# Kernel optimization log

Hardware: AMD Instinct MI355X
Metric: run time of the kernel (lower is better)

The kernel has to match this reference:

```python
import jax, jax.numpy as jnp
import numpy as np
import math
from jax import lax

B, HS, WS, C, T, TD, HH, TOPM = 8, 64, 64, 512, 77, 512, 8, 3
DH = C // HH
CONF_TH = 0.35


def _layernorm(x, w, b, eps=1e-5):
    mu = x.mean(-1, keepdims=True)
    var = ((x - mu) ** 2).mean(-1, keepdims=True)
    return (x - mu) * lax.rsqrt(var + eps) * w + b


def _l2norm(x, eps=1e-6):
    n = jnp.sqrt((x * x).sum(-1, keepdims=True))
    return x / jnp.maximum(n, eps)


def _forward(visual_features, text_features, geo_mask,
             ln1_w, ln1_b, wq, bq, wk, bk, wv, bv, wo, bo,
             gate_w, gate_b, logit_scale, alpha,
             ln2_w, ln2_b, ffn_w1, ffn_b1, ffn_w2, ffn_b2):
    Bb, Hs, Ws, Cv = visual_features.shape
    N = Hs * Ws
    # Pre-LN + flatten spatial
    x = _layernorm(visual_features, ln1_w, ln1_b).reshape(Bb, N, Cv)
    q_full = x @ wq + bq                                  # [B,N,C]
    pad_mask = jnp.abs(text_features).sum(-1) <= 1e-6     # [B,T]
    k_full = text_features @ wk + bk                      # [B,T,C]
    v_full = text_features @ wv + bv
    # per-token L2 normalize over full channel dim, then split heads
    q = _l2norm(q_full).reshape(Bb, N, HH, DH)
    k = _l2norm(k_full).reshape(Bb, T, HH, DH)
    v = v_full.reshape(Bb, T, HH, DH)
    scale = jnp.exp(jnp.clip(logit_scale, -2.0, 2.0)) / jnp.sqrt(jnp.float32(DH))
    sim = jnp.einsum('bnhd,bthd->bnht', q, k) * scale     # [B,N,H,T]
    # geo gate (4D tensor branch): log-bias on logits + multiplicative channel gate later
    gate_map = jnp.clip(geo_mask, 0.3, 1.0)               # [B,1,Hs,Ws]
    geo_gate_flat = gate_map.reshape(Bb, N, 1)            # [B,N,1]
    sim = sim + jnp.log(jnp.maximum(gate_map.reshape(Bb, N), 1e-6))[:, :, None, None]
    sim = jnp.where(pad_mask[:, None, None, :], -jnp.inf, sim)
    # Top-K sparsification before softmax (threshold at the K-th value)
    topv = lax.top_k(sim, TOPM)[0]                        # [B,N,H,K]
    sim = jnp.where(sim >= topv[..., -1:], sim, -jnp.inf)
    attn = jax.nn.softmax(sim, axis=-1)
    attn = attn / jnp.maximum(attn.sum(-1, keepdims=True), 1e-6)
    # fully-padded rows -> zero
    all_pad = pad_mask.all(axis=1)
    attn = jnp.where(all_pad[:, None, None, None], 0.0, attn)
    # confidence bypass: conf = max_prob * (1 - normalized entropy), mean over heads
    a_hn = attn.transpose(0, 2, 1, 3)                     # [B,H,N,T]
    maxp = a_hn.max(-1, keepdims=True)
    t_eff = jnp.maximum((a_hn > 0).astype(a_hn.dtype).sum(-1, keepdims=True), 2.0)
    p = jnp.maximum(a_hn, 1e-8)
    ent = jnp.maximum(-(p * jnp.log(p)).sum(-1, keepdims=True) / jnp.log(t_eff), 0.0)
    conf = jnp.clip(maxp * (1.0 - ent), 0.0, 1.0).mean(axis=1)   # [B,N,1]
    conf_scale = CONF_TH + (1.0 - CONF_TH) * jnp.clip(conf, 0.0, 1.0)
    aligned = jnp.einsum('bnht,bthd->bnhd', attn, v).reshape(Bb, N, HH * DH)
    aligned = (aligned @ wo + bo) * conf_scale
    gate = jax.nn.sigmoid(x @ gate_w + gate_b) * geo_gate_flat
    y = x + alpha * gate * aligned
    h = _layernorm(y, ln2_w, ln2_b)
    y = y + (jax.nn.gelu(h @ ffn_w1 + ffn_b1, approximate=False) @ ffn_w2 + ffn_b2)
    return y.reshape(Bb, Hs, Ws, Cv)


def setup_inputs() -> dict:
    key = jax.random.key(0)
    ks = jax.random.split(key, 16)
    def w(k, shp, fan_in):
        return (jax.random.normal(k, shp, jnp.float32) * (1.0 / math.sqrt(fan_in))).astype(jnp.float32)
    return {
        'visual_features': jax.random.normal(ks[0], (B, HS, WS, C), jnp.float32),
        'text_features':   jax.random.normal(ks[1], (B, T, TD), jnp.float32),
        'geo_mask':        jax.random.uniform(ks[2], (B, 1, HS, WS), jnp.float32),
        'ln1_w': jnp.ones((C,), jnp.float32), 'ln1_b': jnp.zeros((C,), jnp.float32),
        'wq': w(ks[3], (C, C), C),   'bq': jnp.zeros((C,), jnp.float32),
        'wk': w(ks[4], (TD, C), TD), 'bk': jnp.zeros((C,), jnp.float32),
        'wv': w(ks[5], (TD, C), TD), 'bv': jnp.zeros((C,), jnp.float32),
        'wo': w(ks[6], (C, C), C),   'bo': jnp.zeros((C,), jnp.float32),
        'gate_w': w(ks[7], (C, C), C), 'gate_b': jnp.zeros((C,), jnp.float32),
        'logit_scale': jnp.float32(math.log(1.0 / 0.07)),
        'alpha': jnp.float32(0.1),
        'ln2_w': jnp.ones((C,), jnp.float32), 'ln2_b': jnp.zeros((C,), jnp.float32),
        'ffn_w1': w(ks[8], (C, 4 * C), C),    'ffn_b1': jnp.zeros((4 * C,), jnp.float32),
        'ffn_w2': w(ks[9], (4 * C, C), 4 * C), 'ffn_b2': jnp.zeros((C,), jnp.float32),
    }


def reference(visual_features, text_features, geo_mask,
              ln1_w, ln1_b, wq, bq, wk, bk, wv, bv, wo, bo,
              gate_w, gate_b, logit_scale, alpha,
              ln2_w, ln2_b, ffn_w1, ffn_b1, ffn_w2, ffn_b2):
    return _forward(visual_features, text_features, geo_mask,
                    ln1_w, ln1_b, wq, bq, wk, bk, wv, bv, wo, bo,
                    gate_w, gate_b, logit_scale, alpha,
                    ln2_w, ln2_b, ffn_w1, ffn_b1, ffn_w2, ffn_b2)
```

## Files before the change

kernel.cpp:

```cpp
#include <hip/hip_runtime.h>
#include <hip/hip_bf16.h>
#include <math.h>

#define TT 77
#define MTOT 32768

typedef __attribute__((ext_vector_type(8))) short bf16x8;
typedef __attribute__((ext_vector_type(4))) float floatx4;

#define GPTR(p) ((const __attribute__((address_space(1))) void*)(p))
#define LPTR(p) ((__attribute__((address_space(3))) void*)(p))

__device__ __forceinline__ float wred_sum(float v) {
#pragma unroll
  for (int o = 32; o >= 1; o >>= 1) v += __shfl_xor(v, o, 64);
  return v;
}

__device__ __forceinline__ unsigned short f2bf(float f) {
  unsigned int u = __float_as_uint(f);
  unsigned int r = (u + 0x7fffu + ((u >> 16) & 1u)) >> 16;
  return (unsigned short)r;
}
__device__ __forceinline__ float bf2f(unsigned short h) {
  return __uint_as_float(((unsigned int)h) << 16);
}

__device__ __forceinline__ float fast_gelu(float o) {
  const float z = fabsf(o) * 0.70710678118654752f;
  const float t = __builtin_amdgcn_rcpf(fmaf(0.3275911f, z, 1.0f));
  float p = fmaf(1.061405429f, t, -1.453152027f);
  p = fmaf(p, t, 1.421413741f);
  p = fmaf(p, t, -0.284496736f);
  p = fmaf(p, t, 0.254829592f);
  p = p * t;
  const float erfz = fmaf(-p, __expf(-z * z), 1.0f);
  const float s = __builtin_copysignf(erfz, o);
  return 0.5f * o * (1.0f + s);
}

__device__ __forceinline__ float fast_sigmoid(float o) {
  return __builtin_amdgcn_rcpf(1.0f + __expf(-o));
}

__global__ __launch_bounds__(256)
void ln_bf16_kernel(const float* __restrict__ in, const float* __restrict__ gw,
                    const float* __restrict__ gb, unsigned short* __restrict__ out) {
  const int wv = threadIdx.x >> 6, lane = threadIdx.x & 63;
  const size_t row = (size_t)blockIdx.x * 4 + wv;
  const float* p = in + row * 512 + lane * 8;
  float4 a = *(const float4*)p;
  float4 b = *(const float4*)(p + 4);
  float s = a.x + a.y + a.z + a.w + b.x + b.y + b.z + b.w;
  float mu = wred_sum(s) * (1.0f / 512.0f);
  float d[8] = {a.x - mu, a.y - mu, a.z - mu, a.w - mu,
                b.x - mu, b.y - mu, b.z - mu, b.w - mu};
  float ss = 0.f;
#pragma unroll
  for (int i = 0; i < 8; ++i) ss = fmaf(d[i], d[i], ss);
  float var = wred_sum(ss) * (1.0f / 512.0f);
  float rstd = rsqrtf(var + 1e-5f);
  float4 w0 = *(const float4*)(gw + lane * 8);
  float4 w1 = *(const float4*)(gw + lane * 8 + 4);
  float4 c0 = *(const float4*)(gb + lane * 8);
  float4 c1 = *(const float4*)(gb + lane * 8 + 4);
  float o[8];
  o[0] = d[0] * rstd * w0.x + c0.x;  o[1] = d[1] * rstd * w0.y + c0.y;
  o[2] = d[2] * rstd * w0.z + c0.z;  o[3] = d[3] * rstd * w0.w + c0.w;
  o[4] = d[4] * rstd * w1.x + c1.x;  o[5] = d[5] * rstd * w1.y + c1.y;
  o[6] = d[6] * rstd * w1.z + c1.z;  o[7] = d[7] * rstd * w1.w + c1.w;
  __align__(16) unsigned short ob[8];
#pragma unroll
  for (int i = 0; i < 8; ++i) ob[i] = f2bf(o[i]);
  *(uint4*)(out + row * 512 + lane * 8) = *(const uint4*)ob;
}

__global__ __launch_bounds__(256)
void qnorm_kernel(const float* __restrict__ q, const float* __restrict__ logit_scale,
                  unsigned short* __restrict__ qnb) {
  const int wv = threadIdx.x >> 6, lane = threadIdx.x & 63;
  const size_t row = (size_t)blockIdx.x * 4 + wv;
  const float ls = fminf(fmaxf(logit_scale[0], -2.0f), 2.0f);
  const float scale = expf(ls) * 0.125f;
  const float* p = q + row * 512 + lane * 8;
  float4 a = *(const float4*)p;
  float4 b = *(const float4*)(p + 4);
  float ss = a.x * a.x + a.y * a.y + a.z * a.z + a.w * a.w +
             b.x * b.x + b.y * b.y + b.z * b.z + b.w * b.w;
  ss = wred_sum(ss);
  const float nsc = scale / fmaxf(sqrtf(ss), 1e-6f);
  float o[8] = {a.x * nsc, a.y * nsc, a.z * nsc, a.w * nsc,
                b.x * nsc, b.y * nsc, b.z * nsc, b.w * nsc};
  __align__(16) unsigned short ob[8];
#pragma unroll
  for (int i = 0; i < 8; ++i) ob[i] = f2bf(o[i]);
  *(uint4*)(qnb + row * 512 + lane * 8) = *(const uint4*)ob;
}

__global__ __launch_bounds__(256)
void transpose_bf16_kernel(const float* __restrict__ W, unsigned short* __restrict__ WTb,
                           int K, int N) {
  __shared__ float s[32][33];
  const int tx = threadIdx.x & 31, ty = threadIdx.x >> 5;
  const int n0 = blockIdx.x * 32, k0 = blockIdx.y * 32;
#pragma unroll
  for (int j = 0; j < 4; ++j)
    s[ty + 8 * j][tx] = W[(size_t)(k0 + ty + 8 * j) * N + n0 + tx];
  __syncthreads();
#pragma unroll
  for (int j = 0; j < 4; ++j)
    WTb[(size_t)(n0 + ty + 8 * j) * K + k0 + tx] = f2bf(s[tx][ty + 8 * j]);
}

__global__ __launch_bounds__(256)
void transpose_pair_kernel(const float* __restrict__ W,
                           unsigned short* __restrict__ WTh,
                           unsigned short* __restrict__ WTl, int K, int N) {
  __shared__ float s[32][33];
  const int tx = threadIdx.x & 31, ty = threadIdx.x >> 5;
  const int n0 = blockIdx.x * 32, k0 = blockIdx.y * 32;
#pragma unroll
  for (int j = 0; j < 4; ++j)
    s[ty + 8 * j][tx] = W[(size_t)(k0 + ty + 8 * j) * N + n0 + tx];
  __syncthreads();
#pragma unroll
  for (int j = 0; j < 4; ++j) {
    const float a = s[tx][ty + 8 * j];
    const unsigned short hi = f2bf(a);
    WTh[(size_t)(n0 + ty + 8 * j) * K + k0 + tx] = hi;
    WTl[(size_t)(n0 + ty + 8 * j) * K + k0 + tx] = f2bf(a - bf2f(hi));
  }
}

__global__ __launch_bounds__(256)
void text_cvt_kernel(const float* __restrict__ text,
                     unsigned short* __restrict__ thi,
                     unsigned short* __restrict__ tlo,
                     float* __restrict__ negm) {
  const int wv = threadIdx.x >> 6, lane = threadIdx.x & 63;
  const int row = blockIdx.x * 4 + wv;
  if (row >= 616) {
    const uint4 z = {0u, 0u, 0u, 0u};
    *(uint4*)(thi + (size_t)row * 512 + lane * 8) = z;
    *(uint4*)(tlo + (size_t)row * 512 + lane * 8) = z;
    return;
  }
  const float* p = text + (size_t)row * 512 + lane * 8;
  float4 a = *(const float4*)p;
  float4 b = *(const float4*)(p + 4);
  float v[8] = {a.x, a.y, a.z, a.w, b.x, b.y, b.z, b.w};
  float ab = 0.f;
#pragma unroll
  for (int i = 0; i < 8; ++i) ab += fabsf(v[i]);
  ab = wred_sum(ab);
  __align__(16) unsigned short hb[8];
  __align__(16) unsigned short lb[8];
#pragma unroll
  for (int i = 0; i < 8; ++i) {
    hb[i] = f2bf(v[i]);
    lb[i] = f2bf(v[i] - bf2f(hb[i]));
  }
  *(uint4*)(thi + (size_t)row * 512 + lane * 8) = *(const uint4*)hb;
  *(uint4*)(tlo + (size_t)row * 512 + lane * 8) = *(const uint4*)lb;
  if (lane == 0) {
    const int bb = row / 77, t = row - bb * 77;
    negm[bb * 80 + t] = (ab <= 1e-6f) ? -INFINITY : 0.0f;
  }
}

__global__ __launch_bounds__(256)
void kv_gemm(const unsigned short* __restrict__ AH,
             const unsigned short* __restrict__ AL,
             const unsigned short* __restrict__ BH,
             const unsigned short* __restrict__ BL,
             const float* __restrict__ bk, const float* __restrict__ bv,
             float* __restrict__ outp) {
  const int K = 512;
  __shared__ __align__(16) unsigned short AsH[128 * 32];
  __shared__ __align__(16) unsigned short AsL[128 * 32];
  __shared__ __align__(16) unsigned short BsH[128 * 32];
  __shared__ __align__(16) unsigned short BsL[128 * 32];
  const int tid = threadIdx.x;
  const int wid = tid >> 6, lane = tid & 63;
  const int wr = wid >> 1, wc = wid & 1;
  const int m16 = lane & 15, quad = lane >> 4;
  const int row0 = blockIdx.y * 128, col0 = blockIdx.x * 128;

  const floatx4 zero4 = {0.f, 0.f, 0.f, 0.f};
  floatx4 acc[4][4];
#pragma unroll
  for (int i = 0; i < 4; ++i)
#pragma unroll
    for (int j = 0; j < 4; ++j) acc[i][j] = zero4;

  const int srow = tid >> 2;
  const int schunk = (tid & 3) ^ (srow & 3);
  const unsigned short* AgH = AH + (size_t)(row0 + srow) * K + schunk * 8;
  const unsigned short* AgL = AL + (size_t)(row0 + srow) * K + schunk * 8;
  const unsigned short* BgH = BH + (size_t)(col0 + srow) * K + schunk * 8;
  const unsigned short* BgL = BL + (size_t)(col0 + srow) * K + schunk * 8;
  char* AsHB = (char*)AsH + tid * 16;
  char* AsLB = (char*)AsL + tid * 16;
  char* BsHB = (char*)BsH + tid * 16;
  char* BsLB = (char*)BsL + tid * 16;
  const int rq = quad ^ (m16 & 3);
  const int aOfs = (wr * 64 + m16) * 32 + rq * 8;
  const int bOfs = (wc * 64 + m16) * 32 + rq * 8;

  for (int k0 = 0; k0 < K; k0 += 32) {
    __syncthreads();
    __builtin_amdgcn_global_load_lds(GPTR(AgH + k0), LPTR(AsHB), 16, 0, 0);
    __builtin_amdgcn_global_load_lds(GPTR(AgH + (size_t)64 * K + k0), LPTR(AsHB + 4096), 16, 0, 0);
    __builtin_amdgcn_global_load_lds(GPTR(AgL + k0), LPTR(AsLB), 16, 0, 0);
    __builtin_amdgcn_global_load_lds(GPTR(AgL + (size_t)64 * K + k0), LPTR(AsLB + 4096), 16, 0, 0);
    __builtin_amdgcn_global_load_lds(GPTR(BgH + k0), LPTR(BsHB), 16, 0, 0);
    __builtin_amdgcn_global_load_lds(GPTR(BgH + (size_t)64 * K + k0), LPTR(BsHB + 4096), 16, 0, 0);
    __builtin_amdgcn_global_load_lds(GPTR(BgL + k0), LPTR(BsLB), 16, 0, 0);
    __builtin_amdgcn_global_load_lds(GPTR(BgL + (size_t)64 * K + k0), LPTR(BsLB + 4096), 16, 0, 0);
    __syncthreads();
    bf16x8 afH[4], afL[4], bfH[4], bfL[4];
#pragma unroll
    for (int i = 0; i < 4; ++i) {
      afH[i] = *(const bf16x8*)(AsH + aOfs + i * 16 * 32);
      afL[i] = *(const bf16x8*)(AsL + aOfs + i * 16 * 32);
      bfH[i] = *(const bf16x8*)(BsH + bOfs + i * 16 * 32);
      bfL[i] = *(const bf16x8*)(BsL + bOfs + i * 16 * 32);
    }
#pragma unroll
    for (int mi = 0; mi < 4; ++mi)
#pragma unroll
      for (int ni = 0; ni < 4; ++ni) {
        acc[mi][ni] = __builtin_amdgcn_mfma_f32_16x16x32_bf16(afH[mi], bfH[ni], acc[mi][ni], 0, 0, 0);
        acc[mi][ni] = __builtin_amdgcn_mfma_f32_16x16x32_bf16(afH[mi], bfL[ni], acc[mi][ni], 0, 0, 0);
        acc[mi][ni] = __builtin_amdgcn_mfma_f32_16x16x32_bf16(afL[mi], bfH[ni], acc[mi][ni], 0, 0, 0);
      }
  }

  const float* bp = (col0 < 512) ? bk : bv;
  const int cbase = (col0 < 512) ? col0 : col0 - 512;
  float bb[4];
#pragma unroll
  for (int ni = 0; ni < 4; ++ni) bb[ni] = bp[cbase + wc * 64 + ni * 16 + m16];
#pragma unroll
  for (int mi = 0; mi < 4; ++mi)
#pragma unroll
    for (int r = 0; r < 4; ++r) {
      const int row = row0 + wr * 64 + mi * 16 + quad * 4 + r;
#pragma unroll
      for (int ni = 0; ni < 4; ++ni) {
        const int col = col0 + wc * 64 + ni * 16 + m16;
        outp[(size_t)row * 1024 + col] = acc[mi][ni][r] + bb[ni];
      }
    }
}

__global__ __launch_bounds__(256)
void knorm_kernel(const float* __restrict__ KV,
                  unsigned short* __restrict__ khb) {
  const int wv = threadIdx.x >> 6, lane = threadIdx.x & 63;
  const int row = blockIdx.x * 4 + wv;
  const float* p = KV + (size_t)row * 1024 + lane * 8;
  float4 a = *(const float4*)p;
  float4 b = *(const float4*)(p + 4);
  float v[8] = {a.x, a.y, a.z, a.w, b.x, b.y, b.z, b.w};
  float ss = 0.f;
#pragma unroll
  for (int i = 0; i < 8; ++i) ss = fmaf(v[i], v[i], ss);
  ss = wred_sum(ss);
  const float sc = 1.0f / fmaxf(sqrtf(ss), 1e-6f);
  const int bb = row / 77, t = row - bb * 77;
  const int c = lane * 8, h = c >> 6, d = c & 63;
  __align__(16) unsigned short ob[8];
#pragma unroll
  for (int i = 0; i < 8; ++i) ob[i] = f2bf(v[i] * sc);
  *(uint4*)(khb + (((size_t)bb * 8 + h) * 80 + t) * 64 + d) = *(const uint4*)ob;
}

__global__ __launch_bounds__(256)
void kpad_zero_kernel(unsigned short* __restrict__ khb, float* __restrict__ negm) {
  const int i = blockIdx.x * 256 + threadIdx.x;
  const int bh = i / 192, rem = i - bh * 192;
  const int t = 77 + rem / 64, d = rem & 63;
  khb[(((size_t)bh) * 80 + t) * 64 + d] = 0;
  if (i < 24) negm[(i / 3) * 80 + 77 + (i % 3)] = -INFINITY;
}

__global__ __launch_bounds__(256)
void sim_kernel(const unsigned short* __restrict__ qnb,
                const unsigned short* __restrict__ khb,
                const float* __restrict__ negm,
                float* __restrict__ SIM) {
  __shared__ __align__(16) unsigned short As[128 * 72];
  __shared__ __align__(16) unsigned short Bs[80 * 72];
  const int bh = blockIdx.y;
  const int b = bh >> 3, h = bh & 7;
  const int row0 = blockIdx.x * 128;
  const int tid = threadIdx.x;
  {
    const int r = tid >> 1, half = tid & 1;
    const unsigned short* src = qnb + ((size_t)b * 4096 + row0 + r) * 512 + h * 64 + half * 32;
    unsigned short* dst = As + r * 72 + half * 32;
    *(uint4*)dst = *(const uint4*)src;
    *(uint4*)(dst + 8) = *(const uint4*)(src + 8);
    *(uint4*)(dst + 16) = *(const uint4*)(src + 16);
    *(uint4*)(dst + 24) = *(const uint4*)(src + 24);
  }
  if (tid < 160) {
    const int r = tid >> 1, half = tid & 1;
    const unsigned short* src = khb + ((size_t)bh * 80 + r) * 64 + half * 32;
    unsigned short* dst = Bs + r * 72 + half * 32;
    *(uint4*)dst = *(const uint4*)src;
    *(uint4*)(dst + 8) = *(const uint4*)(src + 8);
    *(uint4*)(dst + 16) = *(const uint4*)(src + 16);
    *(uint4*)(dst + 24) = *(const uint4*)(src + 24);
  }
  __syncthreads();
  const int w = tid >> 6, lane = tid & 63;
  const int m16 = lane & 15, quad = lane >> 4;
  const unsigned short* aBase = As + (w * 32 + m16) * 72 + quad * 8;
  const unsigned short* bBase = Bs + m16 * 72 + quad * 8;
  bf16x8 af[2][2], bf[5][2];
#pragma unroll
  for (int mi = 0; mi < 2; ++mi)
#pragma unroll
    for (int kk = 0; kk < 2; ++kk)
      af[mi][kk] = *(const bf16x8*)(aBase + mi * 16 * 72 + kk * 32);
#pragma unroll
  for (int ni = 0; ni < 5; ++ni)
#pragma unroll
    for (int kk = 0; kk < 2; ++kk)
      bf[ni][kk] = *(const bf16x8*)(bBase + ni * 16 * 72 + kk * 32);
  const floatx4 zero4 = {0.f, 0.f, 0.f, 0.f};
  floatx4 acc[2][5];
#pragma unroll
  for (int mi = 0; mi < 2; ++mi)
#pragma unroll
    for (int ni = 0; ni < 5; ++ni) acc[mi][ni] = zero4;
#pragma unroll
  for (int kk = 0; kk < 2; ++kk)
#pragma unroll
    for (int mi = 0; mi < 2; ++mi)
#pragma unroll
      for (int ni = 0; ni < 5; ++ni)
        acc[mi][ni] = __builtin_amdgcn_mfma_f32_16x16x32_bf16(af[mi][kk], bf[ni][kk], acc[mi][ni], 0, 0, 0);
  float nm[5];
#pragma unroll
  for (int ni = 0; ni < 5; ++ni) nm[ni] = negm[b * 80 + ni * 16 + m16];
  float* obase = SIM + ((size_t)bh * 4096 + row0 + w * 32 + quad * 4) * 80 + m16;
#pragma unroll
  for (int mi = 0; mi < 2; ++mi)
#pragma unroll
    for (int ni = 0; ni < 5; ++ni)
#pragma unroll
      for (int r = 0; r < 4; ++r)
        obase[(size_t)(mi * 16 + r) * 80 + ni * 16] = acc[mi][ni][r] + nm[ni];
}

__global__ __launch_bounds__(256)
void attn_topk_pv_kernel(const float* __restrict__ SIM,
                         const float* __restrict__ vf,
                         unsigned short* __restrict__ alignedb,
                         float* __restrict__ conf_out) {
  const int g = blockIdx.x * 256 + threadIdx.x;
  const int b = g >> 15;
  const int local = g & 32767;
  const int n = local >> 3, h = local & 7;
  const float* sp = SIM + ((size_t)(b * 8 + h) * 4096 + n) * 80;

  float m1 = -INFINITY, m2 = -INFINITY, m3 = -INFINITY, m4 = -INFINITY;
  int a1 = 0, a2 = 0, a3 = 0;
#pragma unroll
  for (int i = 0; i < 20; ++i) {
    const float4 q = ((const float4*)sp)[i];
#pragma unroll
    for (int j = 0; j < 4; ++j) {
      const float v = (j == 0) ? q.x : (j == 1) ? q.y : (j == 2) ? q.z : q.w;
      const int t = i * 4 + j;
      const bool c1 = v > m1, c2 = v > m2, c3 = v > m3, c4 = v > m4;
      m4 = c4 ? (c3 ? m3 : v) : m4;
      m3 = c3 ? (c2 ? m2 : v) : m3;
      a3 = c3 ? (c2 ? a2 : t) : a3;
      m2 = c2 ? (c1 ? m1 : v) : m2;
      a2 = c2 ? (c1 ? a1 : t) : a2;
      m1 = c1 ? v : m1;
      a1 = c1 ? t : a1;
    }
  }

  const bool dead = (m1 == -INFINITY);
  if (dead) m1 = 0.0f;
  const bool tie = (!dead) && ((m1 == m2) || (m2 == m3) || (m3 == m4));

  const float d2 = m2 - m1, d3 = m3 - m1;
  const float e2 = __expf(d2), e3 = __expf(d3);
  float s0 = 1.0f + e2 + e3;
  float s1 = ((e2 > 0.f) ? e2 * d2 : 0.f) + ((e3 > 0.f) ? e3 * d3 : 0.f);
  float cntf = 1.0f + ((e2 > 0.f) ? 1.f : 0.f) + ((e3 > 0.f) ? 1.f : 0.f);

  const float w1 = dead ? 0.f : 1.f;
  const float* v1p = vf + (size_t)(b * 77 + a1) * 1024 + h * 64;
  const float* v2p = vf + (size_t)(b * 77 + a2) * 1024 + h * 64;
  const float* v3p = vf + (size_t)(b * 77 + a3) * 1024 + h * 64;
  float4 acc[16];
#pragma unroll
  for (int i = 0; i < 16; ++i) {
    const float4 x1 = ((const float4*)v1p)[i];
    const float4 x2 = ((const float4*)v2p)[i];
    const float4 x3 = ((const float4*)v3p)[i];
    float4 r;
    r.x = fmaf(e3, x3.x, fmaf(e2, x2.x, w1 * x1.x));
    r.y = fmaf(e3, x3.y, fmaf(e2, x2.y, w1 * x1.y));
    r.z = fmaf(e3, x3.z, fmaf(e2, x2.z, w1 * x1.z));
    r.w = fmaf(e3, x3.w, fmaf(e2, x2.w, w1 * x1.w));
    acc[i] = r;
  }

  if (__any(tie)) {
    if (tie) {
      s0 = 0.f; s1 = 0.f; cntf = 0.f;
#pragma unroll
      for (int i = 0; i < 16; ++i) acc[i] = (float4){0.f, 0.f, 0.f, 0.f};
      for (int t = 0; t < 80; ++t) {
        const float v = sp[t];
        if (v >= m3) {
          const float e = expf(v - m1);
          if (e > 0.f) {
            s0 += e; s1 = fmaf(e, v - m1, s1); cntf += 1.f;
            const float4* vp = (const float4*)(vf + (size_t)(b * 77 + t) * 1024 + h * 64);
#pragma unroll
            for (int i = 0; i < 16; ++i) {
              const float4 x = vp[i];
              acc[i].x = fmaf(e, x.x, acc[i].x);
              acc[i].y = fmaf(e, x.y, acc[i].y);
              acc[i].z = fmaf(e, x.z, acc[i].z);
              acc[i].w = fmaf(e, x.w, acc[i].w);
            }
          }
        }
      }
    }
  }

  const float inv = 1.0f / s0;
  const float entn = (__logf(s0) - s1 * inv) + (77.0f - cntf) * 1.8420681e-7f;
  const float ent = fmaxf(entn / __logf(fmaxf(cntf, 2.0f)), 0.0f);
  float conf_h = fminf(fmaxf(inv * (1.0f - ent), 0.0f), 1.0f);
  if (dead) conf_h = 0.f;
  float cs = conf_h;
  cs += __shfl_xor(cs, 1, 64);
  cs += __shfl_xor(cs, 2, 64);
  cs += __shfl_xor(cs, 4, 64);
  if (h == 0) {
    const float cm = fminf(fmaxf(cs * 0.125f, 0.0f), 1.0f);
    conf_out[(size_t)b * 4096 + n] = 0.35f + 0.65f * cm;
  }

  unsigned short* op = alignedb + ((size_t)b * 4096 + n) * 512 + h * 64;
#pragma unroll
  for (int i = 0; i < 8; ++i) {
    const float4 lo = acc[2 * i], hi = acc[2 * i + 1];
    uint4 pk;
    pk.x = (unsigned int)f2bf(lo.x * inv) | ((unsigned int)f2bf(lo.y * inv) << 16);
    pk.y = (unsigned int)f2bf(lo.z * inv) | ((unsigned int)f2bf(lo.w * inv) << 16);
    pk.z = (unsigned int)f2bf(hi.x * inv) | ((unsigned int)f2bf(hi.y * inv) << 16);
    pk.w = (unsigned int)f2bf(hi.z * inv) | ((unsigned int)f2bf(hi.w * inv) << 16);
    *(uint4*)(op + i * 8) = pk;
  }
}

template <int EPI>
__global__ __launch_bounds__(256)
void mfma_gemm(const unsigned short* __restrict__ A,
               const unsigned short* __restrict__ WT,
               const float* __restrict__ bias,
               void* __restrict__ outv, int M, int N, int K,
               const unsigned short* __restrict__ e0b,
               const float* __restrict__ e1f,
               const float* __restrict__ e2f,
               const float* __restrict__ scf) {
  __shared__ __align__(16) unsigned short As[128 * 32];
  __shared__ __align__(16) unsigned short Bs[128 * 32];
  const int tid = threadIdx.x;
  const int wid = tid >> 6, lane = tid & 63;
  const int wr = wid >> 1, wc = wid & 1;
  const int m16 = lane & 15, quad = lane >> 4;

  const int nwg = gridDim.x * gridDim.y;
  const int orig = blockIdx.y * gridDim.x + blockIdx.x;
  const int qq = nwg >> 3, rr = nwg & 7;
  const int xcd = orig & 7, base = orig >> 3;
  const int logical = (xcd < rr ? xcd * (qq + 1) : rr * (qq + 1) + (xcd - rr) * qq) + base;
  const int bx = logical % gridDim.x, by = logical / gridDim.x;
  const int row0 = by * 128, col0 = bx * 128;

  const floatx4 zero4 = {0.f, 0.f, 0.f, 0.f};
  floatx4 acc[4][4];
#pragma unroll
  for (int i = 0; i < 4; ++i)
#pragma unroll
    for (int j = 0; j < 4; ++j) acc[i][j] = zero4;

  const int srow = tid >> 2;
  const int schunk = (tid & 3) ^ (srow & 3);
  const unsigned short* Ag = A + (size_t)(row0 + srow) * K + schunk * 8;
  const unsigned short* Bg = WT + (size_t)(col0 + srow) * K + schunk * 8;
  char* AsB = (char*)As + tid * 16;
  char* BsB = (char*)Bs + tid * 16;
  const int rq = quad ^ (m16 & 3);
  const unsigned short* aP = As + (wr * 64 + m16) * 32 + rq * 8;
  const unsigned short* bP = Bs + (wc * 64 + m16) * 32 + rq * 8;

  for (int k0 = 0; k0 < K; k0 += 32) {
    __syncthreads();
    __builtin_amdgcn_global_load_lds(GPTR(Ag + k0), LPTR(AsB), 16, 0, 0);
    __builtin_amdgcn_global_load_lds(GPTR(Ag + (size_t)64 * K + k0), LPTR(AsB + 4096), 16, 0, 0);
    __builtin_amdgcn_global_load_lds(GPTR(Bg + k0), LPTR(BsB), 16, 0, 0);
    __builtin_amdgcn_global_load_lds(GPTR(Bg + (size_t)64 * K + k0), LPTR(BsB + 4096), 16, 0, 0);
    __syncthreads();
    bf16x8 af[4], bfr[4];
#pragma unroll
    for (int i = 0; i < 4; ++i) {
      af[i] = *(const bf16x8*)(aP + i * 16 * 32);
      bfr[i] = *(const bf16x8*)(bP + i * 16 * 32);
    }
#pragma unroll
    for (int mi = 0; mi < 4; ++mi)
#pragma unroll
      for (int ni = 0; ni < 4; ++ni)
        acc[mi][ni] = __builtin_amdgcn_mfma_f32_16x16x32_bf16(af[mi], bfr[ni], acc[mi][ni], 0, 0, 0);
  }

  float* outf = (float*)outv;
  unsigned short* outb = (unsigned short*)outv;
  const unsigned short* albf = (const unsigned short*)e1f;
  float bb[4];
#pragma unroll
  for (int ni = 0; ni < 4; ++ni) bb[ni] = bias[col0 + wc * 64 + ni * 16 + m16];
  const float alphav = (EPI == 2) ? scf[0] : 0.f;

#pragma unroll
  for (int mi = 0; mi < 4; ++mi) {
#pragma unroll
    for (int r = 0; r < 4; ++r) {
      const int row = row0 + wr * 64 + mi * 16 + quad * 4 + r;
      float rowscale = 1.f, geo = 0.f;
      if (EPI == 1) rowscale = e1f[row];
      if (EPI == 2) geo = fminf(fmaxf(e2f[row], 0.3f), 1.0f);
#pragma unroll
      for (int ni = 0; ni < 4; ++ni) {
        const int col = col0 + wc * 64 + ni * 16 + m16;
        const size_t idx = (size_t)row * N + col;
        float o = acc[mi][ni][r] + bb[ni];
        if (EPI == 0) {
          outf[idx] = o;
        } else if (EPI == 1) {
          outb[idx] = f2bf(o * rowscale);
        } else if (EPI == 2) {
          const float x = bf2f(e0b[idx]);
          const float al = bf2f(albf[idx]);
          const float sg = fast_sigmoid(o);
          outf[idx] = x + alphav * sg * geo * al;
        } else if (EPI == 3) {
          outb[idx] = f2bf(fast_gelu(o));
        } else {
          outf[idx] = o + e1f[idx];
        }
      }
    }
  }
}

extern "C" void kernel_launch(void* const* d_in, const int* in_sizes, int n_in,
                              void* d_out, int out_size, void* d_ws, size_t ws_size,
                              hipStream_t stream) {
  const float* visual = (const float*)d_in[0];
  const float* text   = (const float*)d_in[1];
  const float* geo    = (const float*)d_in[2];
  const float* ln1_w  = (const float*)d_in[3];
  const float* ln1_b  = (const float*)d_in[4];
  const float* wq     = (const float*)d_in[5];
  const float* bq     = (const float*)d_in[6];
  const float* wk     = (const float*)d_in[7];
  const float* bk     = (const float*)d_in[8];
  const float* wvw    = (const float*)d_in[9];
  const float* bv     = (const float*)d_in[10];
  const float* wo     = (const float*)d_in[11];
  const float* bo     = (const float*)d_in[12];
  const float* gate_w = (const float*)d_in[13];
  const float* gate_b = (const float*)d_in[14];
  const float* logit_scale = (const float*)d_in[15];
  const float* alpha  = (const float*)d_in[16];
  const float* ln2_w  = (const float*)d_in[17];
  const float* ln2_b  = (const float*)d_in[18];
  const float* ffn_w1 = (const float*)d_in[19];
  const float* ffn_b1 = (const float*)d_in[20];
  const float* ffn_w2 = (const float*)d_in[21];
  const float* ffn_b2 = (const float*)d_in[22];
  float* out = (float*)d_out;

  char* ws = (char*)d_ws;
  float* R0            = (float*)ws;
  float* BUF2          = (float*)(ws + 88080384);
  unsigned short* Xb   = (unsigned short*)(ws + 155189248);
  unsigned short* QNb  = (unsigned short*)(ws + 188743680);
  unsigned short* wqT  = (unsigned short*)(ws + 222298112);
  unsigned short* woT  = wqT + 262144;
  unsigned short* gateT = woT + 262144;
  unsigned short* w1T  = gateT + 262144;
  unsigned short* w2T  = w1T + 1048576;
  unsigned short* KHb  = w2T + 1048576;
  float* NEGM = (float*)(ws + 230146048);
  float* CONF = (float*)(ws + 230148608);

  float* KV            = (float*)(ws + 88080384);
  unsigned short* THi  = (unsigned short*)(ws + 88080384 + 2621440);
  unsigned short* TLo  = THi + 640 * 512;
  unsigned short* WKVh = TLo + 640 * 512;
  unsigned short* WKVl = WKVh + 1024 * 512;

  float* Qf = R0;
  float* SIM = R0;
  unsigned short* AOb = (unsigned short*)R0;
  unsigned short* ALb = QNb;

  transpose_bf16_kernel<<<dim3(16, 16), 256, 0, stream>>>(wq, wqT, 512, 512);
  transpose_bf16_kernel<<<dim3(16, 16), 256, 0, stream>>>(wo, woT, 512, 512);
  transpose_bf16_kernel<<<dim3(16, 16), 256, 0, stream>>>(gate_w, gateT, 512, 512);
  transpose_bf16_kernel<<<dim3(64, 16), 256, 0, stream>>>(ffn_w1, w1T, 512, 2048);
  transpose_bf16_kernel<<<dim3(16, 64), 256, 0, stream>>>(ffn_w2, w2T, 2048, 512);
  transpose_pair_kernel<<<dim3(16, 16), 256, 0, stream>>>(wk, WKVh, WKVl, 512, 512);
  transpose_pair_kernel<<<dim3(16, 16), 256, 0, stream>>>(wvw, WKVh + 512 * 512, WKVl + 512 * 512, 512, 512);

  ln_bf16_kernel<<<MTOT / 4, 256, 0, stream>>>(visual, ln1_w, ln1_b, Xb);
  text_cvt_kernel<<<160, 256, 0, stream>>>(text, THi, TLo, NEGM);
  kv_gemm<<<dim3(8, 5), 256, 0, stream>>>(THi, TLo, WKVh, WKVl, bk, bv, KV);
  knorm_kernel<<<154, 256, 0, stream>>>(KV, KHb);
  kpad_zero_kernel<<<48, 256, 0, stream>>>(KHb, NEGM);
  mfma_gemm<0><<<dim3(4, 256), 256, 0, stream>>>(Xb, wqT, bq, Qf, MTOT, 512, 512,
                                                 nullptr, nullptr, nullptr, nullptr);
  qnorm_kernel<<<MTOT / 4, 256, 0, stream>>>(Qf, logit_scale, QNb);
  sim_kernel<<<dim3(32, 64), 256, 0, stream>>>(QNb, KHb, NEGM, SIM);
  attn_topk_pv_kernel<<<1024, 256, 0, stream>>>(SIM, KV + 512, ALb, CONF);
  mfma_gemm<1><<<dim3(4, 256), 256, 0, stream>>>(ALb, woT, bo, AOb, MTOT, 512, 512,
                                                 nullptr, CONF, nullptr, nullptr);
  mfma_gemm<2><<<dim3(4, 256), 256, 0, stream>>>(Xb, gateT, gate_b, BUF2, MTOT, 512, 512,
                                                 Xb, (const float*)AOb, geo, alpha);
  ln_bf16_kernel<<<MTOT / 4, 256, 0, stream>>>(BUF2, ln2_w, ln2_b, Xb);
  unsigned short* GCH = (unsigned short*)R0;
  for (int ch = 0; ch < 2; ++ch) {
    const size_t off = (size_t)ch * 16384;
    mfma_gemm<3><<<dim3(16, 128), 256, 0, stream>>>(Xb + off * 512, w1T, ffn_b1, GCH,
                                                    16384, 2048, 512,
                                                    nullptr, nullptr, nullptr, nullptr);
    mfma_gemm<4><<<dim3(4, 128), 256, 0, stream>>>(GCH, w2T, ffn_b2, out + off * 512,
                                                   16384, 512, 2048,
                                                   nullptr, BUF2 + off * 512, nullptr, nullptr);
  }
}
```

Baseline: 631.9 us.

## Fuse Q L2-norm into Q GEMM epilogue and sim scaling, compile-time K

The Q projection GEMM now writes bf16 output directly and accumulates per-row sums of squares with atomics. The sim kernel applies the normalization and logit scale to its accumulators, so the fp32 Q buffer and the separate qnorm pass are removed. The change also makes K a template constant in the GEMM and uses packed bf16 conversion instructions in the epilogues. In exchange, it normalizes unnormalized bf16 Q after rounding, which shifts precision slightly. It also adds atomics and an extra zeroing kernel.

Measured after the change: 606.2 us. 1.04x faster.

```diff
diff --git a/kernel.cpp b/kernel.cpp
--- a/kernel.cpp
+++ b/kernel.cpp
@@ -24,6 +24,11 @@
 }
 __device__ __forceinline__ float bf2f(unsigned short h) {
   return __uint_as_float(((unsigned int)h) << 16);
+}
+__device__ __forceinline__ unsigned int cvt2bf(float a, float b) {
+  unsigned int r;
+  asm("v_cvt_pk_bf16_f32 %0, %1, %2" : "=v"(r) : "v"(a), "v"(b));
+  return r;
 }
 
 __device__ __forceinline__ float fast_gelu(float o) {
@@ -76,25 +81,8 @@
 }
 
 __global__ __launch_bounds__(256)
-void qnorm_kernel(const float* __restrict__ q, const float* __restrict__ logit_scale,
-                  unsigned short* __restrict__ qnb) {
-  const int wv = threadIdx.x >> 6, lane = threadIdx.x & 63;
-  const size_t row = (size_t)blockIdx.x * 4 + wv;
-  const float ls = fminf(fmaxf(logit_scale[0], -2.0f), 2.0f);
-  const float scale = expf(ls) * 0.125f;
-  const float* p = q + row * 512 + lane * 8;
-  float4 a = *(const float4*)p;
-  float4 b = *(const float4*)(p + 4);
-  float ss = a.x * a.x + a.y * a.y + a.z * a.z + a.w * a.w +
-             b.x * b.x + b.y * b.y + b.z * b.z + b.w * b.w;
-  ss = wred_sum(ss);
-  const float nsc = scale / fmaxf(sqrtf(ss), 1e-6f);
-  float o[8] = {a.x * nsc, a.y * nsc, a.z * nsc, a.w * nsc,
-                b.x * nsc, b.y * nsc, b.z * nsc, b.w * nsc};
-  __align__(16) unsigned short ob[8];
-#pragma unroll
-  for (int i = 0; i < 8; ++i) ob[i] = f2bf(o[i]);
-  *(uint4*)(qnb + row * 512 + lane * 8) = *(const uint4*)ob;
+void zero_ss_kernel(float* __restrict__ ssq) {
+  ssq[blockIdx.x * 256 + threadIdx.x] = 0.0f;
 }
 
 __global__ __launch_bounds__(256)
@@ -289,6 +277,8 @@
 void sim_kernel(const unsigned short* __restrict__ qnb,
                 const unsigned short* __restrict__ khb,
                 const float* __restrict__ negm,
+                const float* __restrict__ ssq,
+                const float* __restrict__ logit_scale,
                 float* __restrict__ SIM) {
   __shared__ __align__(16) unsigned short As[128 * 72];
   __shared__ __align__(16) unsigned short Bs[80 * 72];
@@ -343,6 +333,8 @@
 #pragma unroll
       for (int ni = 0; ni < 5; ++ni)
         acc[mi][ni] = __builtin_amdgcn_mfma_f32_16x16x32_bf16(af[mi][kk], bf[ni][kk], acc[mi][ni], 0, 0, 0);
+  const float ls = fminf(fmaxf(logit_scale[0], -2.0f), 2.0f);
+  const float scale = expf(ls) * 0.125f;
   float nm[5];
 #pragma unroll
   for (int ni = 0; ni < 5; ++ni) nm[ni] = negm[b * 80 + ni * 16 + m16];
@@ -350,10 +342,14 @@
 #pragma unroll
   for (int mi = 0; mi < 2; ++mi)
 #pragma unroll
-    for (int ni = 0; ni < 5; ++ni)
-#pragma unroll
-      for (int r = 0; r < 4; ++r)
-        obase[(size_t)(mi * 16 + r) * 80 + ni * 16] = acc[mi][ni][r] + nm[ni];
+    for (int r = 0; r < 4; ++r) {
+      const int rl = row0 + w * 32 + quad * 4 + mi * 16 + r;
+      const float ssv = ssq[(size_t)b * 4096 + rl];
+      const float nsc = scale / fmaxf(sqrtf(ssv), 1e-6f);
+#pragma unroll
+      for (int ni = 0; ni < 5; ++ni)
+        obase[(size_t)(mi * 16 + r) * 80 + ni * 16] = acc[mi][ni][r] * nsc + nm[ni];
+    }
 }
 
 __global__ __launch_bounds__(256)
@@ -460,20 +456,20 @@
   for (int i = 0; i < 8; ++i) {
     const float4 lo = acc[2 * i], hi = acc[2 * i + 1];
     uint4 pk;
-    pk.x = (unsigned int)f2bf(lo.x * inv) | ((unsigned int)f2bf(lo.y * inv) << 16);
-    pk.y = (unsigned int)f2bf(lo.z * inv) | ((unsigned int)f2bf(lo.w * inv) << 16);
-    pk.z = (unsigned int)f2bf(hi.x * inv) | ((unsigned int)f2bf(hi.y * inv) << 16);
-    pk.w = (unsigned int)f2bf(hi.z * inv) | ((unsigned int)f2bf(hi.w * inv) << 16);
+    pk.x = cvt2bf(lo.x * inv, lo.y * inv);
+    pk.y = cvt2bf(lo.z * inv, lo.w * inv);
+    pk.z = cvt2bf(hi.x * inv, hi.y * inv);
+    pk.w = cvt2bf(hi.z * inv, hi.w * inv);
     *(uint4*)(op + i * 8) = pk;
   }
 }
 
-template <int EPI>
+template <int EPI, int KC>
 __global__ __launch_bounds__(256)
 void mfma_gemm(const unsigned short* __restrict__ A,
                const unsigned short* __restrict__ WT,
                const float* __restrict__ bias,
-               void* __restrict__ outv, int M, int N, int K,
+               void* __restrict__ outv, int M, int N,
                const unsigned short* __restrict__ e0b,
                const float* __restrict__ e1f,
                const float* __restrict__ e2f,
@@ -502,20 +498,20 @@
 
   const int srow = tid >> 2;
   const int schunk = (tid & 3) ^ (srow & 3);
-  const unsigned short* Ag = A + (size_t)(row0 + srow) * K + schunk * 8;
-  const unsigned short* Bg = WT + (size_t)(col0 + srow) * K + schunk * 8;
+  const unsigned short* Ag = A + (size_t)(row0 + srow) * KC + schunk * 8;
+  const unsigned short* Bg = WT + (size_t)(col0 + srow) * KC + schunk * 8;
   char* AsB = (char*)As + tid * 16;
   char* BsB = (char*)Bs + tid * 16;
   const int rq = quad ^ (m16 & 3);
   const unsigned short* aP = As + (wr * 64 + m16) * 32 + rq * 8;
   const unsigned short* bP = Bs + (wc * 64 + m16) * 32 + rq * 8;
 
-  for (int k0 = 0; k0 < K; k0 += 32) {
+  for (int k0 = 0; k0 < KC; k0 += 32) {
     __syncthreads();
     __builtin_amdgcn_global_load_lds(GPTR(Ag + k0), LPTR(AsB), 16, 0, 0);
-    __builtin_amdgcn_global_load_lds(GPTR(Ag + (size_t)64 * K + k0), LPTR(AsB + 4096), 16, 0, 0);
+    __builtin_amdgcn_global_load_lds(GPTR(Ag + (size_t)64 * KC + k0), LPTR(AsB + 4096), 16, 0, 0);
     __builtin_amdgcn_global_load_lds(GPTR(Bg + k0), LPTR(BsB), 16, 0, 0);
-    __builtin_amdgcn_global_load_lds(GPTR(Bg + (size_t)64 * K + k0), LPTR(BsB + 4096), 16, 0, 0);
+    __builtin_amdgcn_global_load_lds(GPTR(Bg + (size_t)64 * KC + k0), LPTR(BsB + 4096), 16, 0, 0);
     __syncthreads();
     bf16x8 af[4], bfr[4];
 #pragma unroll
@@ -543,27 +539,54 @@
 #pragma unroll
     for (int r = 0; r < 4; ++r) {
       const int row = row0 + wr * 64 + mi * 16 + quad * 4 + r;
-      float rowscale = 1.f, geo = 0.f;
-      if (EPI == 1) rowscale = e1f[row];
-      if (EPI == 2) geo = fminf(fmaxf(e2f[row], 0.3f), 1.0f);
-#pragma unroll
-      for (int ni = 0; ni < 4; ++ni) {
-        const int col = col0 + wc * 64 + ni * 16 + m16;
-        const size_t idx = (size_t)row * N + col;
-        float o = acc[mi][ni][r] + bb[ni];
-        if (EPI == 0) {
-          outf[idx] = o;
-        } else if (EPI == 1) {
-          outb[idx] = f2bf(o * rowscale);
-        } else if (EPI == 2) {
+      float o[4];
+#pragma unroll
+      for (int ni = 0; ni < 4; ++ni) o[ni] = acc[mi][ni][r] + bb[ni];
+      const size_t basei = (size_t)row * N + col0 + wc * 64 + m16;
+
+      if (EPI == 5) {
+        const unsigned int p01 = cvt2bf(o[0], o[1]);
+        const unsigned int p23 = cvt2bf(o[2], o[3]);
+        outb[basei] = (unsigned short)p01;
+        outb[basei + 16] = (unsigned short)(p01 >> 16);
+        outb[basei + 32] = (unsigned short)p23;
+        outb[basei + 48] = (unsigned short)(p23 >> 16);
+        float p = fmaf(o[0], o[0], fmaf(o[1], o[1], fmaf(o[2], o[2], o[3] * o[3])));
+        p += __shfl_xor(p, 1, 64);
+        p += __shfl_xor(p, 2, 64);
+        p += __shfl_xor(p, 4, 64);
+        p += __shfl_xor(p, 8, 64);
+        if (m16 == 0) atomicAdd(const_cast<float*>(e1f) + row, p);
+      } else if (EPI == 3) {
+        const unsigned int p01 = cvt2bf(fast_gelu(o[0]), fast_gelu(o[1]));
+        const unsigned int p23 = cvt2bf(fast_gelu(o[2]), fast_gelu(o[3]));
+        outb[basei] = (unsigned short)p01;
+        outb[basei + 16] = (unsigned short)(p01 >> 16);
+        outb[basei + 32] = (unsigned short)p23;
+        outb[basei + 48] = (unsigned short)(p23 >> 16);
+      } else if (EPI == 1) {
+        const float rowscale = e1f[row];
+        const unsigned int p01 = cvt2bf(o[0] * rowscale, o[1] * rowscale);
+        const unsigned int p23 = cvt2bf(o[2] * rowscale, o[3] * rowscale);
+        outb[basei] = (unsigned short)p01;
+        outb[basei + 16] = (unsigned short)(p01 >> 16);
+        outb[basei + 32] = (unsigned short)p23;
+        outb[basei + 48] = (unsigned short)(p23 >> 16);
+      } else if (EPI == 2) {
+        const float geo = fminf(fmaxf(e2f[row], 0.3f), 1.0f);
+#pragma unroll
+        for (int ni = 0; ni < 4; ++ni) {
+          const size_t idx = basei + ni * 16;
           const float x = bf2f(e0b[idx]);
           const float al = bf2f(albf[idx]);
-          const float sg = fast_sigmoid(o);
+          const float sg = fast_sigmoid(o[ni]);
           outf[idx] = x + alphav * sg * geo * al;
-        } else if (EPI == 3) {
-          outb[idx] = f2bf(fast_gelu(o));
-        } else {
-          outf[idx] = o + e1f[idx];
+        }
+      } else {
+#pragma unroll
+        for (int ni = 0; ni < 4; ++ni) {
+          const size_t idx = basei + ni * 16;
+          outf[idx] = o[ni] + e1f[idx];
         }
       }
     }
@@ -611,6 +634,7 @@
   unsigned short* KHb  = w2T + 1048576;
   float* NEGM = (float*)(ws + 230146048);
   float* CONF = (float*)(ws + 230148608);
+  float* SSQ  = (float*)(ws + 230279680);
 
   float* KV            = (float*)(ws + 88080384);
   unsigned short* THi  = (unsigned short*)(ws + 88080384 + 2621440);
@@ -618,9 +642,7 @@
   unsigned short* WKVh = TLo + 640 * 512;
   unsigned short* WKVl = WKVh + 1024 * 512;
 
-  float* Qf = R0;
   float* SIM = R0;
-  unsigned short* AOb = (unsigned short*)R0;
   unsigned short* ALb = QNb;
 
   transpose_bf16_kernel<<<dim3(16, 16), 256, 0, stream>>>(wq, wqT, 512, 512);
@@ -632,28 +654,29 @@
   transpose_pair_kernel<<<dim3(16, 16), 256, 0, stream>>>(wvw, WKVh + 512 * 512, WKVl + 512 * 512, 512, 512);
 
   ln_bf16_kernel<<<MTOT / 4, 256, 0, stream>>>(visual, ln1_w, ln1_b, Xb);
+  zero_ss_kernel<<<128, 256, 0, stream>>>(SSQ);
   text_cvt_kernel<<<160, 256, 0, stream>>>(text, THi, TLo, NEGM);
   kv_gemm<<<dim3(8, 5), 256, 0, stream>>>(THi, TLo, WKVh, WKVl, bk, bv, KV);
   knorm_kernel<<<154, 256, 0, stream>>>(KV, KHb);
   kpad_zero_kernel<<<48, 256, 0, stream>>>(KHb, NEGM);
-  mfma_gemm<0><<<dim3(4, 256), 256, 0, stream>>>(Xb, wqT, bq, Qf, MTOT, 512, 512,
-                                                 nullptr, nullptr, nullptr, nullptr);
-  qnorm_kernel<<<MTOT / 4, 256, 0, stream>>>(Qf, logit_scale, QNb);
-  sim_kernel<<<dim3(32, 64), 256, 0, stream>>>(QNb, KHb, NEGM, SIM);
+  mfma_gemm<5, 512><<<dim3(4, 256), 256, 0, stream>>>(Xb, wqT, bq, QNb, MTOT, 512,
+                                                      nullptr, SSQ, nullptr, nullptr);
+  sim_kernel<<<dim3(32, 64), 256, 0, stream>>>(QNb, KHb, NEGM, SSQ, logit_scale, SIM);
   attn_topk_pv_kernel<<<1024, 256, 0, stream>>>(SIM, KV + 512, ALb, CONF);
-  mfma_gemm<1><<<dim3(4, 256), 256, 0, stream>>>(ALb, woT, bo, AOb, MTOT, 512, 512,
-                                                 nullptr, CONF, nullptr, nullptr);
-  mfma_gemm<2><<<dim3(4, 256), 256, 0, stream>>>(Xb, gateT, gate_b, BUF2, MTOT, 512, 512,
-                                                 Xb, (const float*)AOb, geo, alpha);
+  unsigned short* AOb = (unsigned short*)R0;
+  mfma_gemm<1, 512><<<dim3(4, 256), 256, 0, stream>>>(ALb, woT, bo, AOb, MTOT, 512,
+                                                      nullptr, CONF, nullptr, nullptr);
+  mfma_gemm<2, 512><<<dim3(4, 256), 256, 0, stream>>>(Xb, gateT, gate_b, BUF2, MTOT, 512,
+                                                      Xb, (const float*)AOb, geo, alpha);
   ln_bf16_kernel<<<MTOT / 4, 256, 0, stream>>>(BUF2, ln2_w, ln2_b, Xb);
   unsigned short* GCH = (unsigned short*)R0;
   for (int ch = 0; ch < 2; ++ch) {
     const size_t off = (size_t)ch * 16384;
-    mfma_gemm<3><<<dim3(16, 128), 256, 0, stream>>>(Xb + off * 512, w1T, ffn_b1, GCH,
-                                                    16384, 2048, 512,
-                                                    nullptr, nullptr, nullptr, nullptr);
-    mfma_gemm<4><<<dim3(4, 128), 256, 0, stream>>>(GCH, w2T, ffn_b2, out + off * 512,
-                                                   16384, 512, 2048,
-                                                   nullptr, BUF2 + off * 512, nullptr, nullptr);
-  }
-}
+    mfma_gemm<3, 512><<<dim3(16, 128), 256, 0, stream>>>(Xb + off * 512, w1T, ffn_b1, GCH,
+                                                         16384, 2048,
+                                                         nullptr, nullptr, nullptr, nullptr);
+    mfma_gemm<4, 2048><<<dim3(4, 128), 256, 0, stream>>>(GCH, w2T, ffn_b2, out + off * 512,
+                                                         16384, 512,
+                                                         nullptr, BUF2 + off * 512, nullptr, nullptr);
+  }
+}
```
